# Kernel tuning notes

Measured on AMD Instinct MI355X. Metric: run time of the kernel, lower is better.

The kernel has to match this reference:

```python
import math
import jax, jax.numpy as jnp
import numpy as np

D_IN, R_S, T_MAX = 1024, 256, 2048
B, T = 8, 2048


def setup_inputs() -> dict:
    key = jax.random.key(0)
    ks = jax.random.split(key, 8)
    u = jax.random.normal(ks[0], (B, T, D_IN), dtype=jnp.float32)
    h0_r = jax.random.normal(ks[1], (B, R_S), dtype=jnp.float32)
    h0_i = jax.random.normal(ks[2], (B, R_S), dtype=jnp.float32)
    # parameters (lambda_raw randomized instead of zeros so sigmoid is nontrivial)
    lambda_raw = jax.random.normal(ks[3], (R_S,), dtype=jnp.float32)
    # omega init exactly as in the torch module
    log_min, log_max = math.log(1.0 / T_MAX), math.log(math.pi)
    n = np.arange(1, R_S + 1, dtype=np.float32)
    weyl_freqs = n * math.pi / R_S
    log_freqs = np.exp(np.linspace(log_min, log_max, R_S, dtype=np.float32))
    omega = jnp.asarray(0.5 * weyl_freqs + 0.5 * log_freqs, dtype=jnp.float32)
    W_proj = jax.random.normal(ks[4], (R_S, D_IN), dtype=jnp.float32) / math.sqrt(D_IN)
    W_res = jax.random.normal(ks[5], (2 * R_S, D_IN), dtype=jnp.float32) / math.sqrt(D_IN)
    ln_gamma = jnp.ones((2 * R_S,), dtype=jnp.float32)
    ln_beta = jnp.zeros((2 * R_S,), dtype=jnp.float32)
    return {"u": u, "h0_r": h0_r, "h0_i": h0_i, "lambda_raw": lambda_raw,
            "omega": omega, "W_proj": W_proj, "W_res": W_res,
            "ln_gamma": ln_gamma, "ln_beta": ln_beta}


def _layernorm(x, gamma, beta, eps=1e-5):
    mu = jnp.mean(x, axis=-1, keepdims=True)
    var = jnp.mean(jnp.square(x - mu), axis=-1, keepdims=True)
    return (x - mu) * jax.lax.rsqrt(var + eps) * gamma + beta


def reference(u, h0_r, h0_i, lambda_raw, omega, W_proj, W_res, ln_gamma, ln_beta):
    Bb, Tt, _ = u.shape
    lam = -jax.nn.sigmoid(lambda_raw) * 5.0                      # [R]
    t = jnp.arange(Tt, dtype=jnp.float32)                        # [T]
    decay = jnp.exp(lam[:, None] * t[None, :])                   # [R,T]
    phase = omega[:, None] * t[None, :]                          # [R,T]
    f_r = decay * jnp.cos(phase)
    f_i = decay * jnp.sin(phase)
    u_proj = jnp.einsum('btd,rd->brt', u, W_proj)                # [B,R,T]
    n_fft = 2 * Tt
    U_f = jnp.fft.rfft(u_proj, n=n_fft, axis=-1)                 # [B,R,F]
    F_r = jnp.fft.rfft(f_r, n=n_fft, axis=-1)[None]              # [1,R,F]
    F_i = jnp.fft.rfft(f_i, n=n_fft, axis=-1)[None]
    h_r = jnp.fft.irfft(U_f * F_r, n=n_fft, axis=-1)[..., :Tt]   # [B,R,T]
    h_i = jnp.fft.irfft(U_f * F_i, n=n_fft, axis=-1)[..., :Tt]
    # ZIR correction from initial state
    t_zir = t + 1.0
    decay_z = jnp.exp(lam[:, None] * t_zir[None, :])             # [R,T]
    phase_z = omega[:, None] * t_zir[None, :]
    f_r_z = decay_z * jnp.cos(phase_z)
    f_i_z = decay_z * jnp.sin(phase_z)
    h0r = h0_r[:, :, None]                                       # [B,R,1]
    h0i = h0_i[:, :, None]
    h_r = h_r + h0r * f_r_z[None] - h0i * f_i_z[None]
    h_i = h_i + h0r * f_i_z[None] + h0i * f_r_z[None]
    h_r = jnp.swapaxes(h_r, 1, 2)                                # [B,T,R]
    h_i = jnp.swapaxes(h_i, 1, 2)
    ssm_out = jnp.concatenate([h_r, h_i], axis=-1)               # [B,T,2R]
    res = jnp.einsum('btd,ed->bte', u, W_res)                    # [B,T,2R]
    out = _layernorm(ssm_out + res, ln_gamma, ln_beta)
    final_r = jax.lax.stop_gradient(h_r[:, -1])
    final_i = jax.lax.stop_gradient(h_i[:, -1])
    return out, final_r, final_i
```

## Files before the change

kernel.cpp:

```cpp
#include <hip/hip_runtime.h>
#include <math.h>

#define T_LEN 2048
#define BB    8
#define RS    256
#define DIN   1024
#define NE    768
#define M_TOT (BB * T_LEN)
#define LCH   32
#define NCH   (T_LEN / LCH)
#define OUT_MAIN (M_TOT * 512)

typedef unsigned short ushort;
typedef unsigned int   uint;
typedef short  short8  __attribute__((ext_vector_type(8)));
typedef float  f32x16  __attribute__((ext_vector_type(16)));
typedef ushort ushort8 __attribute__((ext_vector_type(8)));

__device__ __forceinline__ ushort f2bf_rn(float x) {
    uint u = __float_as_uint(x);
    return (ushort)((u + 0x7FFFu + ((u >> 16) & 1u)) >> 16);
}
__device__ __forceinline__ float bf2f(ushort b) {
    return __uint_as_float(((uint)b) << 16);
}

__device__ __forceinline__ void gload16(const ushort* g, ushort* l) {
    __builtin_amdgcn_global_load_lds(
        (const __attribute__((address_space(1))) uint*)g,
        (__attribute__((address_space(3))) uint*)l, 16, 0, 0);
}

#define N8U  (M_TOT * DIN / 8)
#define N8WP (RS * DIN / 8)
#define N8WR (2 * RS * DIN / 8)
#define N8TOT (N8U + N8WP + N8WR)

__global__ __launch_bounds__(256) void split_kernel(
    const float* __restrict__ u, const float* __restrict__ wp,
    const float* __restrict__ wr, ushort* __restrict__ Uhi,
    ushort* __restrict__ Ulo, ushort* __restrict__ Whi, ushort* __restrict__ Wlo)
{
    const int i = blockIdx.x * 256 + threadIdx.x;
    if (i >= N8TOT) return;
    const float* src; ushort* hi; ushort* lo; int j;
    if (i < N8U)              { src = u;  hi = Uhi; lo = Ulo; j = i; }
    else if (i < N8U + N8WP)  { src = wp; hi = Whi; lo = Wlo; j = i - N8U; }
    else                      { src = wr; hi = Whi + (size_t)RS * DIN;
                                lo = Wlo + (size_t)RS * DIN; j = i - N8U - N8WP; }
    const float4 x0 = ((const float4*)src)[(size_t)j * 2 + 0];
    const float4 x1 = ((const float4*)src)[(size_t)j * 2 + 1];
    const float xs[8] = {x0.x, x0.y, x0.z, x0.w, x1.x, x1.y, x1.z, x1.w};
    ushort8 hv, lv;
#pragma unroll
    for (int k = 0; k < 8; ++k) {
        const ushort hb = f2bf_rn(xs[k]);
        hv[k] = hb;
        lv[k] = f2bf_rn(xs[k] - bf2f(hb));
    }
    ((ushort8*)hi)[j] = hv;
    ((ushort8*)lo)[j] = lv;
}

#define BKK 32
#define KTILES (DIN / BKK)

__global__ __launch_bounds__(256) void gemm_mfma(
    const ushort* __restrict__ Uh, const ushort* __restrict__ Ul,
    const ushort* __restrict__ Wh, const ushort* __restrict__ Wl,
    float* __restrict__ C)
{
    __shared__ ushort lds[2][4][4096];
    const int tid  = threadIdx.x;
    const int id   = blockIdx.x;
    const int sid  = (id & 7) * 96 + (id >> 3);
    const int bn   = sid % 6;
    const int bm   = sid / 6;
    const int wid  = tid >> 6;
    const int lane = tid & 63;
    const int wr   = wid >> 1, wc = wid & 1;
    const int l31  = lane & 31;
    const int lh   = lane >> 5;

    const int srow = tid & 127;
    const int kb0  = tid >> 7;
    const size_t arow = (size_t)(bm * 128 + srow) * DIN + kb0 * 8;
    const size_t brow = (size_t)(bn * 128 + srow) * DIN + kb0 * 8;
    const ushort* gsrc[4] = { Uh + arow, Ul + arow, Wh + brow, Wl + brow };
    const int lslot0 = tid * 8;
    const int lslot1 = (256 + tid) * 8;

    f32x16 acc[2][2];
#pragma unroll
    for (int m = 0; m < 2; ++m)
#pragma unroll
        for (int n = 0; n < 2; ++n)
#pragma unroll
            for (int j = 0; j < 16; ++j) acc[m][n][j] = 0.f;

#pragma unroll
    for (int p = 0; p < 4; ++p) {
        gload16(gsrc[p],      &lds[0][p][lslot0]);
        gload16(gsrc[p] + 16, &lds[0][p][lslot1]);
    }
    __syncthreads();

    int bufc = 0;
    for (int kt = 0; kt < KTILES; ++kt) {
        const int kk = kt * BKK;
        if (kt + 1 < KTILES) {
#pragma unroll
            for (int p = 0; p < 4; ++p) {
                gload16(gsrc[p] + kk + BKK,      &lds[bufc ^ 1][p][lslot0]);
                gload16(gsrc[p] + kk + BKK + 16, &lds[bufc ^ 1][p][lslot1]);
            }
        }
#pragma unroll
        for (int t2 = 0; t2 < 2; ++t2) {
            const int kblk = t2 * 2 + lh;
            short8 ah[2], al[2], bh[2], bl[2];
#pragma unroll
            for (int m = 0; m < 2; ++m) {
                const int row = wr * 64 + m * 32 + l31;
                ah[m] = *(const short8*)&lds[bufc][0][kblk * 1024 + row * 8];
                al[m] = *(const short8*)&lds[bufc][1][kblk * 1024 + row * 8];
            }
#pragma unroll
            for (int n = 0; n < 2; ++n) {
                const int col = wc * 64 + n * 32 + l31;
                bh[n] = *(const short8*)&lds[bufc][2][kblk * 1024 + col * 8];
                bl[n] = *(const short8*)&lds[bufc][3][kblk * 1024 + col * 8];
            }
#pragma unroll
            for (int m = 0; m < 2; ++m)
#pragma unroll
                for (int n = 0; n < 2; ++n) {
                    acc[m][n] = __builtin_amdgcn_mfma_f32_32x32x16_bf16(ah[m], bh[n], acc[m][n], 0, 0, 0);
                    acc[m][n] = __builtin_amdgcn_mfma_f32_32x32x16_bf16(ah[m], bl[n], acc[m][n], 0, 0, 0);
                    acc[m][n] = __builtin_amdgcn_mfma_f32_32x32x16_bf16(al[m], bh[n], acc[m][n], 0, 0, 0);
                }
        }
        __syncthreads();
        bufc ^= 1;
    }

    const int crow0 = bm * 128 + wr * 64;
    const int ccol0 = bn * 128 + wc * 64 + l31;
#pragma unroll
    for (int m = 0; m < 2; ++m)
#pragma unroll
        for (int n = 0; n < 2; ++n) {
            const int col = ccol0 + n * 32;
#pragma unroll
            for (int j = 0; j < 16; ++j) {
                const int row = crow0 + m * 32 + (j & 3) + 8 * (j >> 2) + 4 * lh;
                C[(size_t)row * NE + col] = acc[m][n][j];
            }
        }
}

__device__ inline void pole(const float* __restrict__ lraw, const float* __restrict__ om,
                            int r, float& zr, float& zi, float& lam, float& o)
{
    const float x   = lraw[r];
    const float sig = 1.f / (1.f + expf(-x));
    lam = -5.f * sig;
    o   = om[r];
    const float er = expf(lam);
    zr = er * cosf(o);
    zi = er * sinf(o);
}

__global__ __launch_bounds__(256) void carry_kernel(
    const float* __restrict__ C, const float* __restrict__ lraw,
    const float* __restrict__ om, float2* __restrict__ carry)
{
    const int c = blockIdx.x, b = blockIdx.y, r = threadIdx.x;
    const int m0 = b * T_LEN + c * LCH;
    float zr, zi, lam, o;
    pole(lraw, om, r, zr, zi, lam, o);
    const float* p = C + (size_t)m0 * NE + r;
    float hr = 0.f, hi = 0.f;
#pragma unroll 8
    for (int s = 0; s < LCH; ++s) {
        const float u  = p[(size_t)s * NE];
        const float nr = zr * hr - zi * hi + u;
        const float ni = zr * hi + zi * hr;
        hr = nr; hi = ni;
    }
    carry[(size_t)(b * NCH + c) * RS + r] = make_float2(hr, hi);
}

__global__ __launch_bounds__(256) void chunk_scan_kernel(
    const float2* __restrict__ carry, const float* __restrict__ h0r,
    const float* __restrict__ h0i, const float* __restrict__ lraw,
    const float* __restrict__ om, float2* __restrict__ S, float* __restrict__ out)
{
    const int b = blockIdx.x, r = threadIdx.x;
    __shared__ float2 cs[32 * RS];
    float zr, zi, lam, o;
    pole(lraw, om, r, zr, zi, lam, o);
    const float eL  = expf(lam * (float)LCH);
    const float zLr = eL * cosf(o * (float)LCH);
    const float zLi = eL * sinf(o * (float)LCH);
    float sr = h0r[b * RS + r];
    float si = h0i[b * RS + r];
    for (int half = 0; half < 2; ++half) {
        __syncthreads();
        const float4* src = (const float4*)(carry + ((size_t)b * NCH + half * 32) * RS);
        float4* dst = (float4*)cs;
        for (int i = r; i < 32 * RS / 2; i += 256) dst[i] = src[i];
        __syncthreads();
        for (int cc = 0; cc < 32; ++cc) {
            const int c = half * 32 + cc;
            S[((size_t)b * NCH + c) * RS + r] = make_float2(sr, si);
            const float2 k = cs[cc * RS + r];
            const float nr = zLr * sr - zLi * si + k.x;
            const float ni = zLr * si + zLi * sr + k.y;
            sr = nr; si = ni;
        }
    }
    out[OUT_MAIN + b * RS + r]           = sr;
    out[OUT_MAIN + BB * RS + b * RS + r] = si;
}

__global__ __launch_bounds__(256) void scan_ln_kernel(
    const float* __restrict__ C, const float2* __restrict__ S,
    const float* __restrict__ lraw, const float* __restrict__ om,
    const float* __restrict__ gamma, const float* __restrict__ beta,
    float* __restrict__ out)
{
    const int c = blockIdx.x, b = blockIdx.y, r = threadIdx.x;
    __shared__ float xt[8][512];
    const int m0 = b * T_LEN + c * LCH;
    float zr, zi, lam, o;
    pole(lraw, om, r, zr, zi, lam, o);
    float2 st = S[(size_t)(b * NCH + c) * RS + r];
    const int wid = r >> 6, lane = r & 63;
    const float4 g0  = *(const float4*)&gamma[lane * 8];
    const float4 g1  = *(const float4*)&gamma[lane * 8 + 4];
    const float4 be0 = *(const float4*)&beta[lane * 8];
    const float4 be1 = *(const float4*)&beta[lane * 8 + 4];

    for (int batch = 0; batch < 4; ++batch) {
        const int s0 = batch * 8;
#pragma unroll
        for (int s = 0; s < 8; ++s) {
            const int m = m0 + s0 + s;
            const float u  = C[(size_t)m * NE + r];
            const float hr = zr * st.x - zi * st.y + u;
            const float hi = zr * st.y + zi * st.x;
            st.x = hr; st.y = hi;
            xt[s][r]       = hr + C[(size_t)m * NE + 256 + r];
            xt[s][256 + r] = hi + C[(size_t)m * NE + 512 + r];
        }
        __syncthreads();
#pragma unroll
        for (int rr = 0; rr < 2; ++rr) {
            const int s = wid * 2 + rr;
            const int m = m0 + s0 + s;
            const float4 x0 = *(const float4*)&xt[s][lane * 8];
            const float4 x1 = *(const float4*)&xt[s][lane * 8 + 4];
            float s1 = (x0.x + x0.y) + (x0.z + x0.w) + (x1.x + x1.y) + (x1.z + x1.w);
            float s2 = (x0.x * x0.x + x0.y * x0.y) + (x0.z * x0.z + x0.w * x0.w)
                     + (x1.x * x1.x + x1.y * x1.y) + (x1.z * x1.z + x1.w * x1.w);
#pragma unroll
            for (int off = 1; off < 64; off <<= 1) {
                s1 += __shfl_xor(s1, off);
                s2 += __shfl_xor(s2, off);
            }
            const float mu   = s1 * (1.f / 512.f);
            const float var  = s2 * (1.f / 512.f) - mu * mu;
            const float rstd = rsqrtf(var + 1e-5f);
            float4 o0, o1;
            o0.x = (x0.x - mu) * rstd * g0.x + be0.x;
            o0.y = (x0.y - mu) * rstd * g0.y + be0.y;
            o0.z = (x0.z - mu) * rstd * g0.z + be0.z;
            o0.w = (x0.w - mu) * rstd * g0.w + be0.w;
            o1.x = (x1.x - mu) * rstd * g1.x + be1.x;
            o1.y = (x1.y - mu) * rstd * g1.y + be1.y;
            o1.z = (x1.z - mu) * rstd * g1.z + be1.z;
            o1.w = (x1.w - mu) * rstd * g1.w + be1.w;
            *(float4*)&out[(size_t)m * 512 + lane * 8]     = o0;
            *(float4*)&out[(size_t)m * 512 + lane * 8 + 4] = o1;
        }
        __syncthreads();
    }
}

extern "C" void kernel_launch(void* const* d_in, const int* in_sizes, int n_in,
                              void* d_out, int out_size, void* d_ws, size_t ws_size,
                              hipStream_t stream)
{
    const float* u    = (const float*)d_in[0];
    const float* h0r  = (const float*)d_in[1];
    const float* h0i  = (const float*)d_in[2];
    const float* lraw = (const float*)d_in[3];
    const float* omg  = (const float*)d_in[4];
    const float* Wp   = (const float*)d_in[5];
    const float* Wr   = (const float*)d_in[6];
    const float* gam  = (const float*)d_in[7];
    const float* bet  = (const float*)d_in[8];
    float* out = (float*)d_out;

    float*  C     = (float*)d_ws;
    float2* carry = (float2*)(C + (size_t)M_TOT * NE);
    float2* S     = carry + (size_t)BB * NCH * RS;
    ushort* Uhi   = (ushort*)(S + (size_t)BB * NCH * RS);
    ushort* Ulo   = Uhi + (size_t)M_TOT * DIN;
    ushort* Whi   = Ulo + (size_t)M_TOT * DIN;
    ushort* Wlo   = Whi + (size_t)NE * DIN;

    split_kernel<<<N8TOT / 256, 256, 0, stream>>>(u, Wp, Wr, Uhi, Ulo, Whi, Wlo);
    gemm_mfma<<<768, 256, 0, stream>>>(Uhi, Ulo, Whi, Wlo, C);
    carry_kernel<<<dim3(NCH, BB), 256, 0, stream>>>(C, lraw, omg, carry);
    chunk_scan_kernel<<<BB, 256, 0, stream>>>(carry, h0r, h0i, lraw, omg, S, out);
    scan_ln_kernel<<<dim3(NCH, BB), 256, 0, stream>>>(C, (const float2*)S, lraw, omg, gam, bet, out);
}
```

Before: 262.8 us.

## Rework GEMM to 16x16 MFMA single-buffered tiles and stage scan rows in LDS

The GEMM drops double-buffered LDS prefetch and the swizzled block mapping in favour of a plain 2D grid, single-buffered 128x128x32 tiles and 16x16x32 bf16 MFMAs. The scan/LayerNorm kernel now loads whole 768-wide rows of C with coalesced float4 reads into a shared tile, prefetching the next batch into registers. That replaces the strided per-element global reads. The GEMM gives up load/compute overlap and L2-friendly block ordering, and it may also hit LDS bank conflicts with a row stride of 32 bf16.

```diff
diff --git a/kernel.cpp b/kernel.cpp
--- a/kernel.cpp
+++ b/kernel.cpp
@@ -14,7 +14,7 @@
 typedef unsigned short ushort;
 typedef unsigned int   uint;
 typedef short  short8  __attribute__((ext_vector_type(8)));
-typedef float  f32x16  __attribute__((ext_vector_type(16)));
+typedef float  f32x4   __attribute__((ext_vector_type(4)));
 typedef ushort ushort8 __attribute__((ext_vector_type(8)));
 
 __device__ __forceinline__ ushort f2bf_rn(float x) {
@@ -62,101 +62,86 @@
     ((ushort8*)lo)[j] = lv;
 }
 
-#define BKK 32
-#define KTILES (DIN / BKK)
+#define Bb 128
+#define BK 32
 
 __global__ __launch_bounds__(256) void gemm_mfma(
     const ushort* __restrict__ Uh, const ushort* __restrict__ Ul,
     const ushort* __restrict__ Wh, const ushort* __restrict__ Wl,
     float* __restrict__ C)
 {
-    __shared__ ushort lds[2][4][4096];
+    __shared__ ushort Ah[Bb * BK], Al[Bb * BK], Bh[Bb * BK], Bl[Bb * BK];
     const int tid  = threadIdx.x;
-    const int id   = blockIdx.x;
-    const int sid  = (id & 7) * 96 + (id >> 3);
-    const int bn   = sid % 6;
-    const int bm   = sid / 6;
+    const int bn   = blockIdx.x;
+    const int bm   = blockIdx.y;
     const int wid  = tid >> 6;
     const int lane = tid & 63;
     const int wr   = wid >> 1, wc = wid & 1;
-    const int l31  = lane & 31;
-    const int lh   = lane >> 5;
-
-    const int srow = tid & 127;
-    const int kb0  = tid >> 7;
-    const size_t arow = (size_t)(bm * 128 + srow) * DIN + kb0 * 8;
-    const size_t brow = (size_t)(bn * 128 + srow) * DIN + kb0 * 8;
-    const ushort* gsrc[4] = { Uh + arow, Ul + arow, Wh + brow, Wl + brow };
-    const int lslot0 = tid * 8;
-    const int lslot1 = (256 + tid) * 8;
-
-    f32x16 acc[2][2];
-#pragma unroll
-    for (int m = 0; m < 2; ++m)
-#pragma unroll
-        for (int n = 0; n < 2; ++n)
-#pragma unroll
-            for (int j = 0; j < 16; ++j) acc[m][n][j] = 0.f;
-
-#pragma unroll
-    for (int p = 0; p < 4; ++p) {
-        gload16(gsrc[p],      &lds[0][p][lslot0]);
-        gload16(gsrc[p] + 16, &lds[0][p][lslot1]);
-    }
-    __syncthreads();
-
-    int bufc = 0;
-    for (int kt = 0; kt < KTILES; ++kt) {
-        const int kk = kt * BKK;
-        if (kt + 1 < KTILES) {
-#pragma unroll
-            for (int p = 0; p < 4; ++p) {
-                gload16(gsrc[p] + kk + BKK,      &lds[bufc ^ 1][p][lslot0]);
-                gload16(gsrc[p] + kk + BKK + 16, &lds[bufc ^ 1][p][lslot1]);
+    const int fr   = lane & 15;
+    const int fq   = lane >> 4;
+
+    const int srow = tid >> 2;
+    const int skk  = (tid & 3) * 8;
+    const ushort* gAh = Uh + (size_t)(bm * 128 + srow) * DIN + skk;
+    const ushort* gAl = Ul + (size_t)(bm * 128 + srow) * DIN + skk;
+    const ushort* gBh = Wh + (size_t)(bn * 128 + srow) * DIN + skk;
+    const ushort* gBl = Wl + (size_t)(bn * 128 + srow) * DIN + skk;
+    ushort* lAh0 = Ah + tid * 8; ushort* lAh1 = Ah + 64 * BK + tid * 8;
+    ushort* lAl0 = Al + tid * 8; ushort* lAl1 = Al + 64 * BK + tid * 8;
+    ushort* lBh0 = Bh + tid * 8; ushort* lBh1 = Bh + 64 * BK + tid * 8;
+    ushort* lBl0 = Bl + tid * 8; ushort* lBl1 = Bl + 64 * BK + tid * 8;
+    const size_t rstep = (size_t)64 * DIN;
+
+    f32x4 acc[4][4];
+#pragma unroll
+    for (int m = 0; m < 4; ++m)
+#pragma unroll
+        for (int n = 0; n < 4; ++n) acc[m][n] = (f32x4){0.f, 0.f, 0.f, 0.f};
+
+    for (int kk = 0; kk < DIN; kk += BK) {
+        gload16(gAh + kk, lAh0); gload16(gAh + kk + rstep, lAh1);
+        gload16(gAl + kk, lAl0); gload16(gAl + kk + rstep, lAl1);
+        gload16(gBh + kk, lBh0); gload16(gBh + kk + rstep, lBh1);
+        gload16(gBl + kk, lBl0); gload16(gBl + kk + rstep, lBl1);
+        __syncthreads();
+
+        short8 ah[4], al[4], bh[4], bl[4];
+#pragma unroll
+        for (int m = 0; m < 4; ++m) {
+            const int row = wr * 64 + m * 16 + fr;
+            ah[m] = *(const short8*)&Ah[row * BK + fq * 8];
+            al[m] = *(const short8*)&Al[row * BK + fq * 8];
+        }
+#pragma unroll
+        for (int n = 0; n < 4; ++n) {
+            const int col = wc * 64 + n * 16 + fr;
+            bh[n] = *(const short8*)&Bh[col * BK + fq * 8];
+            bl[n] = *(const short8*)&Bl[col * BK + fq * 8];
+        }
+#pragma unroll
+        for (int m = 0; m < 4; ++m)
+#pragma unroll
+            for (int n = 0; n < 4; ++n) {
+                acc[m][n] = __builtin_amdgcn_mfma_f32_16x16x32_bf16(ah[m], bh[n], acc[m][n], 0, 0, 0);
+                acc[m][n] = __builtin_amdgcn_mfma_f32_16x16x32_bf16(ah[m], bl[n], acc[m][n], 0, 0, 0);
+                acc[m][n] = __builtin_amdgcn_mfma_f32_16x16x32_bf16(al[m], bh[n], acc[m][n], 0, 0, 0);
             }
-        }
-#pragma unroll
-        for (int t2 = 0; t2 < 2; ++t2) {
-            const int kblk = t2 * 2 + lh;
-            short8 ah[2], al[2], bh[2], bl[2];
-#pragma unroll
-            for (int m = 0; m < 2; ++m) {
-                const int row = wr * 64 + m * 32 + l31;
-                ah[m] = *(const short8*)&lds[bufc][0][kblk * 1024 + row * 8];
-                al[m] = *(const short8*)&lds[bufc][1][kblk * 1024 + row * 8];
-            }
-#pragma unroll
-            for (int n = 0; n < 2; ++n) {
-                const int col = wc * 64 + n * 32 + l31;
-                bh[n] = *(const short8*)&lds[bufc][2][kblk * 1024 + col * 8];
-                bl[n] = *(const short8*)&lds[bufc][3][kblk * 1024 + col * 8];
-            }
-#pragma unroll
-            for (int m = 0; m < 2; ++m)
-#pragma unroll
-                for (int n = 0; n < 2; ++n) {
-                    acc[m][n] = __builtin_amdgcn_mfma_f32_32x32x16_bf16(ah[m], bh[n], acc[m][n], 0, 0, 0);
-                    acc[m][n] = __builtin_amdgcn_mfma_f32_32x32x16_bf16(ah[m], bl[n], acc[m][n], 0, 0, 0);
-                    acc[m][n] = __builtin_amdgcn_mfma_f32_32x32x16_bf16(al[m], bh[n], acc[m][n], 0, 0, 0);
-                }
-        }
-        __syncthreads();
-        bufc ^= 1;
+        __syncthreads();
     }
 
     const int crow0 = bm * 128 + wr * 64;
-    const int ccol0 = bn * 128 + wc * 64 + l31;
-#pragma unroll
-    for (int m = 0; m < 2; ++m)
-#pragma unroll
-        for (int n = 0; n < 2; ++n) {
-            const int col = ccol0 + n * 32;
-#pragma unroll
-            for (int j = 0; j < 16; ++j) {
-                const int row = crow0 + m * 32 + (j & 3) + 8 * (j >> 2) + 4 * lh;
-                C[(size_t)row * NE + col] = acc[m][n][j];
-            }
-        }
+    const int ccol0 = bn * 128 + wc * 64;
+#pragma unroll
+    for (int m = 0; m < 4; ++m) {
+        const int row = crow0 + m * 16 + fq * 4;
+#pragma unroll
+        for (int n = 0; n < 4; ++n) {
+            const int col = ccol0 + n * 16 + fr;
+#pragma unroll
+            for (int j = 0; j < 4; ++j)
+                C[(size_t)(row + j) * NE + col] = acc[m][n][j];
+        }
+    }
 }
 
 __device__ inline void pole(const float* __restrict__ lraw, const float* __restrict__ om,
@@ -231,7 +216,7 @@
     float* __restrict__ out)
 {
     const int c = blockIdx.x, b = blockIdx.y, r = threadIdx.x;
-    __shared__ float xt[8][512];
+    __shared__ float tile[8][NE];
     const int m0 = b * T_LEN + c * LCH;
     float zr, zi, lam, o;
     pole(lraw, om, r, zr, zi, lam, o);
@@ -242,25 +227,38 @@
     const float4 be0 = *(const float4*)&beta[lane * 8];
     const float4 be1 = *(const float4*)&beta[lane * 8 + 4];
 
+    float4 rv[6];
+    {
+        const float4* src = (const float4*)(C + (size_t)m0 * NE);
+#pragma unroll
+        for (int k = 0; k < 6; ++k) rv[k] = src[r + 256 * k];
+#pragma unroll
+        for (int k = 0; k < 6; ++k) ((float4*)tile)[r + 256 * k] = rv[k];
+    }
+
     for (int batch = 0; batch < 4; ++batch) {
-        const int s0 = batch * 8;
+        __syncthreads();
+        if (batch < 3) {
+            const float4* src = (const float4*)(C + (size_t)(m0 + (batch + 1) * 8) * NE);
+#pragma unroll
+            for (int k = 0; k < 6; ++k) rv[k] = src[r + 256 * k];
+        }
 #pragma unroll
         for (int s = 0; s < 8; ++s) {
-            const int m = m0 + s0 + s;
-            const float u  = C[(size_t)m * NE + r];
+            const float u  = tile[s][r];
             const float hr = zr * st.x - zi * st.y + u;
             const float hi = zr * st.y + zi * st.x;
             st.x = hr; st.y = hi;
-            xt[s][r]       = hr + C[(size_t)m * NE + 256 + r];
-            xt[s][256 + r] = hi + C[(size_t)m * NE + 512 + r];
+            tile[s][256 + r] = hr + tile[s][256 + r];
+            tile[s][512 + r] = hi + tile[s][512 + r];
         }
         __syncthreads();
 #pragma unroll
         for (int rr = 0; rr < 2; ++rr) {
             const int s = wid * 2 + rr;
-            const int m = m0 + s0 + s;
-            const float4 x0 = *(const float4*)&xt[s][lane * 8];
-            const float4 x1 = *(const float4*)&xt[s][lane * 8 + 4];
+            const int m = m0 + batch * 8 + s;
+            const float4 x0 = *(const float4*)&tile[s][256 + lane * 8];
+            const float4 x1 = *(const float4*)&tile[s][256 + lane * 8 + 4];
             float s1 = (x0.x + x0.y) + (x0.z + x0.w) + (x1.x + x1.y) + (x1.z + x1.w);
             float s2 = (x0.x * x0.x + x0.y * x0.y) + (x0.z * x0.z + x0.w * x0.w)
                      + (x1.x * x1.x + x1.y * x1.y) + (x1.z * x1.z + x1.w * x1.w);
@@ -285,6 +283,10 @@
             *(float4*)&out[(size_t)m * 512 + lane * 8 + 4] = o1;
         }
         __syncthreads();
+        if (batch < 3) {
+#pragma unroll
+            for (int k = 0; k < 6; ++k) ((float4*)tile)[r + 256 * k] = rv[k];
+        }
     }
 }
 
@@ -312,7 +314,7 @@
     ushort* Wlo   = Whi + (size_t)NE * DIN;
 
     split_kernel<<<N8TOT / 256, 256, 0, stream>>>(u, Wp, Wr, Uhi, Ulo, Whi, Wlo);
-    gemm_mfma<<<768, 256, 0, stream>>>(Uhi, Ulo, Whi, Wlo, C);
+    gemm_mfma<<<dim3(NE / 128, M_TOT / 128), 256, 0, stream>>>(Uhi, Ulo, Whi, Wlo, C);
     carry_kernel<<<dim3(NCH, BB), 256, 0, stream>>>(C, lraw, omg, carry);
     chunk_scan_kernel<<<BB, 256, 0, stream>>>(carry, h0r, h0i, lraw, omg, S, out);
     scan_ln_kernel<<<dim3(NCH, BB), 256, 0, stream>>>(C, (const float2*)S, lraw, omg, gam, bet, out);
```

After: 258.6 us. About the same (-1.6%).
